# Optimization experiments

Measured on AMD Instinct MI355X. Metric: run time of the kernel, lower is better.

Reference implementation:

```python
import jax, jax.numpy as jnp
import numpy as np

N, E, D_IN, D_HID, D_OUT, R, B = 50000, 600000, 128, 128, 128, 8, 4


def setup_inputs() -> dict:
    key = jax.random.key(0)
    ks = jax.random.split(key, 12)
    s = 0.05
    return {
        "x": jax.random.normal(ks[0], (N, D_IN), jnp.float32),
        "edge_index": jax.random.randint(ks[1], (2, E), 0, N, jnp.int32),
        "edge_type": jax.random.randint(ks[2], (E,), 0, R, jnp.int32),
        "basis1": jax.random.normal(ks[3], (B, D_IN, D_HID), jnp.float32) * s,
        "comp1": jax.random.normal(ks[4], (R, B), jnp.float32) * s,
        "root1": jax.random.normal(ks[5], (D_IN, D_HID), jnp.float32) * s,
        "bias1": jnp.zeros((D_HID,), jnp.float32),
        "basis2": jax.random.normal(ks[6], (B, D_HID, D_OUT), jnp.float32) * s,
        "comp2": jax.random.normal(ks[7], (R, B), jnp.float32) * s,
        "root2": jax.random.normal(ks[8], (D_HID, D_OUT), jnp.float32) * s,
        "bias2": jnp.zeros((D_OUT,), jnp.float32),
    }


def _rgcn_conv(x, src, dst, etype, basis, comp, root, bias):
    # PyG RGCNConv (basis decomposition, aggr='mean' per relation):
    # out_i = x_i @ root + bias + sum_r mean_{e: type=r, dst=i} (x_src_e @ W_r)
    # W_r linear => aggregate raw features per (node, relation), then transform.
    n = x.shape[0]
    r = comp.shape[0]
    W = jnp.einsum('rb,bio->rio', comp, basis)          # [R, in, out]
    seg = dst * r + etype                               # [E] composite key
    agg = jax.ops.segment_sum(x[src], seg, num_segments=n * r)        # [N*R, in]
    cnt = jax.ops.segment_sum(jnp.ones_like(seg, x.dtype), seg, num_segments=n * r)
    mean = (agg / jnp.maximum(cnt, 1.0)[:, None]).reshape(n, r, -1)   # [N, R, in]
    return jnp.einsum('nri,rio->no', mean, W) + x @ root + bias


def reference(x, edge_index, edge_type, basis1, comp1, root1, bias1,
              basis2, comp2, root2, bias2):
    src, dst = edge_index[0], edge_index[1]
    h = _rgcn_conv(x, src, dst, edge_type, basis1, comp1, root1, bias1)
    h = jax.nn.relu(h)
    # dropout p=0.2 is identity in eval mode
    out = _rgcn_conv(h, src, dst, edge_type, basis2, comp2, root2, bias2)
    return out
```

## Files before the change

kernel.cpp:

```cpp
#include <hip/hip_runtime.h>

#define NN 50000
#define NE 600000
#define DD 128
#define RR 8
#define NBASIS 4
#define NR (NN * RR)
#define KTOT 640
#define KZ 512
#define MPAD 50048

typedef float f32x4 __attribute__((ext_vector_type(4)));
typedef short bf16x8 __attribute__((ext_vector_type(8)));
typedef unsigned int u32x4 __attribute__((ext_vector_type(4)));

static __device__ __forceinline__ unsigned short f2b(float f) {
  union { float f; unsigned u; } c; c.f = f;
  unsigned u = c.u + 0x7fffu + ((c.u >> 16) & 1u);
  return (unsigned short)(u >> 16);
}
static __device__ __forceinline__ unsigned pack2(float lo, float hi) {
  return (unsigned)f2b(lo) | ((unsigned)f2b(hi) << 16);
}
static __device__ __forceinline__ float b2f_lo(unsigned v) {
  union { unsigned u; float f; } c; c.u = v << 16; return c.f;
}
static __device__ __forceinline__ float b2f_hi(unsigned v) {
  union { unsigned u; float f; } c; c.u = v & 0xffff0000u; return c.f;
}

#define PREP_XB 12500
#define PREP_BT 320
#define PREP_CNT 2344
#define PREP_TOTAL (PREP_XB + 2 * PREP_BT + PREP_CNT)

__global__ __launch_bounds__(256) void prep_kernel(
    const float* __restrict__ x, const float* __restrict__ basis1,
    const float* __restrict__ root1, const float* __restrict__ basis2,
    const float* __restrict__ root2, const int* __restrict__ dst,
    const int* __restrict__ et, unsigned* __restrict__ xb,
    unsigned short* __restrict__ BT1, unsigned short* __restrict__ BT2,
    int* __restrict__ cnt) {
  int bid = blockIdx.x;
  int t = threadIdx.x;
  if (bid < PREP_XB) {
    int i = bid * 256 + t;
    float2 v = ((const float2*)x)[i];
    xb[i] = pack2(v.x, v.y);
  } else if (bid < PREP_XB + PREP_BT) {
    int idx = (bid - PREP_XB) * 256 + t;
    int c = idx / KTOT, k = idx - c * KTOT;
    float v = (k < 512) ? basis1[(size_t)((k >> 7) * DD + (k & 127)) * DD + c]
                        : root1[(size_t)(k - 512) * DD + c];
    BT1[idx] = f2b(v);
  } else if (bid < PREP_XB + 2 * PREP_BT) {
    int idx = (bid - PREP_XB - PREP_BT) * 256 + t;
    int c = idx / KTOT, k = idx - c * KTOT;
    float v = (k < 512) ? basis2[(size_t)((k >> 7) * DD + (k & 127)) * DD + c]
                        : root2[(size_t)(k - 512) * DD + c];
    BT2[idx] = f2b(v);
  } else {
    int e = (bid - PREP_XB - 2 * PREP_BT) * 256 + t;
    if (e < NE) atomicAdd(&cnt[dst[e] * RR + et[e]], 1);
  }
}

__global__ __launch_bounds__(256) void offs_kernel(
    const int* __restrict__ cnt, int2* __restrict__ od,
    int* __restrict__ curs, int* __restrict__ gcur) {
  __shared__ int s[256];
  __shared__ int base;
  int t = threadIdx.x;
  int i = blockIdx.x * 256 + t;
  int v = 0;
  if (i < NN) {
    const int4* c4 = (const int4*)cnt;
    int4 a = c4[i * 2];
    int4 b = c4[i * 2 + 1];
    v = a.x + a.y + a.z + a.w + b.x + b.y + b.z + b.w;
  }
  s[t] = v;
  __syncthreads();
  for (int off = 1; off < 256; off <<= 1) {
    int add = (t >= off) ? s[t - off] : 0;
    __syncthreads();
    s[t] += add;
    __syncthreads();
  }
  if (t == 255) base = atomicAdd(gcur, s[255]);
  __syncthreads();
  if (i < NN) {
    int o = base + s[t] - v;
    od[i] = make_int2(o, v);
    curs[i] = o;
  }
}

__global__ __launch_bounds__(256) void sort_kernel(
    const int* __restrict__ src, const int* __restrict__ dst,
    const int* __restrict__ et, int* __restrict__ curs,
    int* __restrict__ skey) {
  int e = blockIdx.x * 256 + threadIdx.x;
  if (e >= NE) return;
  int p = atomicAdd(&curs[dst[e]], 1);
  skey[p] = src[e] | (et[e] << 28);
}

__global__ __launch_bounds__(256) void agg_kernel(
    const u32x4* __restrict__ featb4,
    const int* __restrict__ skey, const int* __restrict__ cnt,
    const float* __restrict__ comp, const int2* __restrict__ od,
    u32x4* __restrict__ Ab4) {
  __shared__ float ccl[4][RR * NBASIS];
  int tid = threadIdx.x;
  int w = tid >> 6;
  int lane = tid & 63;
  int node = blockIdx.x * 4 + w;
  int g = lane >> 4;
  int q = lane & 15;

  int2 o_d = od[node];
  int beg = o_d.x, dg = o_d.y;

  if (lane < RR * NBASIS) {
    int c = cnt[node * RR + (lane >> 2)];
    ccl[w][lane] = comp[lane] * (1.0f / (float)max(c, 1));
  }
  __syncthreads();

  float a0[8] = {}, a1[8] = {}, a2[8] = {}, a3[8] = {};
  const float4* cc4 = (const float4*)ccl[w];

  for (int i = g; i < dg; i += 8) {
    int p0 = beg + i;
    bool has2 = (i + 4) < dg;
    int p1 = has2 ? p0 + 4 : p0;
    int k0 = skey[p0];
    int k1 = skey[p1];
    u32x4 v0 = featb4[(size_t)(k0 & 0x0FFFFFFF) * 16 + q];
    u32x4 v1 = featb4[(size_t)(k1 & 0x0FFFFFFF) * 16 + q];
    float4 c0 = cc4[((unsigned)k0) >> 28];
    float4 c1 = cc4[((unsigned)k1) >> 28];
    float s1 = has2 ? 1.f : 0.f;
    c1.x *= s1; c1.y *= s1; c1.z *= s1; c1.w *= s1;

    float e[8], f[8];
    e[0] = b2f_lo(v0.x); e[1] = b2f_hi(v0.x);
    e[2] = b2f_lo(v0.y); e[3] = b2f_hi(v0.y);
    e[4] = b2f_lo(v0.z); e[5] = b2f_hi(v0.z);
    e[6] = b2f_lo(v0.w); e[7] = b2f_hi(v0.w);
    f[0] = b2f_lo(v1.x); f[1] = b2f_hi(v1.x);
    f[2] = b2f_lo(v1.y); f[3] = b2f_hi(v1.y);
    f[4] = b2f_lo(v1.z); f[5] = b2f_hi(v1.z);
    f[6] = b2f_lo(v1.w); f[7] = b2f_hi(v1.w);
#pragma unroll
    for (int j = 0; j < 8; ++j) {
      a0[j] += c0.x * e[j] + c1.x * f[j];
      a1[j] += c0.y * e[j] + c1.y * f[j];
      a2[j] += c0.z * e[j] + c1.z * f[j];
      a3[j] += c0.w * e[j] + c1.w * f[j];
    }
  }

#pragma unroll
  for (int j = 0; j < 8; ++j) {
    a0[j] += __shfl_xor(a0[j], 16); a0[j] += __shfl_xor(a0[j], 32);
    a1[j] += __shfl_xor(a1[j], 16); a1[j] += __shfl_xor(a1[j], 32);
    a2[j] += __shfl_xor(a2[j], 16); a2[j] += __shfl_xor(a2[j], 32);
    a3[j] += __shfl_xor(a3[j], 16); a3[j] += __shfl_xor(a3[j], 32);
  }

  u32x4 wv;
  if (g == 0) {
    wv.x = pack2(a0[0], a0[1]); wv.y = pack2(a0[2], a0[3]);
    wv.z = pack2(a0[4], a0[5]); wv.w = pack2(a0[6], a0[7]);
  } else if (g == 1) {
    wv.x = pack2(a1[0], a1[1]); wv.y = pack2(a1[2], a1[3]);
    wv.z = pack2(a1[4], a1[5]); wv.w = pack2(a1[6], a1[7]);
  } else if (g == 2) {
    wv.x = pack2(a2[0], a2[1]); wv.y = pack2(a2[2], a2[3]);
    wv.z = pack2(a2[4], a2[5]); wv.w = pack2(a2[6], a2[7]);
  } else {
    wv.x = pack2(a3[0], a3[1]); wv.y = pack2(a3[2], a3[3]);
    wv.z = pack2(a3[4], a3[5]); wv.w = pack2(a3[6], a3[7]);
  }
  __builtin_nontemporal_store(wv, Ab4 + (size_t)node * 64 + g * 16 + q);
}

template <int OUT_BF16>
__global__ __launch_bounds__(256) void gemm_mfma(
    const unsigned short* __restrict__ Ab,
    const unsigned short* __restrict__ feat,
    const unsigned short* __restrict__ BT,
    const float* __restrict__ bias, void* __restrict__ Cout) {
  __shared__ unsigned short As[128][64];
  __shared__ unsigned short Bs[128][64];

  int tid = threadIdx.x;
  int row0 = blockIdx.x * 128;
  int lane = tid & 63;
  int wid = tid >> 6;
  int wr = (wid >> 1) * 64;
  int wc = (wid & 1) * 64;

  f32x4 acc[4][4] = {};

  for (int kt = 0; kt < KTOT; kt += 64) {
#pragma unroll
    for (int i = 0; i < 4; ++i) {
      int off = i * 256 + tid;
      int r = off >> 3;
      int ke = (off & 7) << 3;
      u32x4 av;
      if (kt < KZ)
        av = __builtin_nontemporal_load(
            (const u32x4*)(Ab + (size_t)(row0 + r) * KZ + kt + ke));
      else
        av = __builtin_nontemporal_load(
            (const u32x4*)(feat + (size_t)(row0 + r) * DD + (kt - KZ) + ke));
      *(u32x4*)((unsigned short*)As + (size_t)off * 8) = av;
      *(u32x4*)((unsigned short*)Bs + (size_t)off * 8) =
          *(const u32x4*)(BT + (size_t)r * KTOT + kt + ke);
    }
    __syncthreads();

#pragma unroll
    for (int kk = 0; kk < 2; ++kk) {
      int ko = kk * 32 + ((lane >> 4) << 3);
      bf16x8 a[4], b[4];
#pragma unroll
      for (int m = 0; m < 4; ++m)
        a[m] = *(const bf16x8*)&As[wr + m * 16 + (lane & 15)][ko];
#pragma unroll
      for (int n = 0; n < 4; ++n)
        b[n] = *(const bf16x8*)&Bs[wc + n * 16 + (lane & 15)][ko];
#pragma unroll
      for (int m = 0; m < 4; ++m)
#pragma unroll
        for (int n = 0; n < 4; ++n)
          acc[m][n] = __builtin_amdgcn_mfma_f32_16x16x32_bf16(
              a[m], b[n], acc[m][n], 0, 0, 0);
    }
    __syncthreads();
  }

#pragma unroll
  for (int n = 0; n < 4; ++n) {
    int col = wc + n * 16 + (lane & 15);
    float bb = bias[col];
#pragma unroll
    for (int m = 0; m < 4; ++m) {
      f32x4 v = acc[m][n];
#pragma unroll
      for (int j = 0; j < 4; ++j) {
        int row = row0 + wr + m * 16 + ((lane >> 4) << 2) + j;
        if (row < NN) {
          float o = v[j] + bb;
          if (OUT_BF16) {
            o = fmaxf(o, 0.f);
            ((unsigned short*)Cout)[(size_t)row * DD + col] = f2b(o);
          } else {
            ((float*)Cout)[(size_t)row * DD + col] = o;
          }
        }
      }
    }
  }
}

extern "C" void kernel_launch(void* const* d_in, const int* in_sizes, int n_in,
                              void* d_out, int out_size, void* d_ws,
                              size_t ws_size, hipStream_t stream) {
  const float* x      = (const float*)d_in[0];
  const int*   eidx   = (const int*)d_in[1];
  const int*   etype  = (const int*)d_in[2];
  const float* basis1 = (const float*)d_in[3];
  const float* comp1  = (const float*)d_in[4];
  const float* root1  = (const float*)d_in[5];
  const float* bias1  = (const float*)d_in[6];
  const float* basis2 = (const float*)d_in[7];
  const float* comp2  = (const float*)d_in[8];
  const float* root2  = (const float*)d_in[9];
  const float* bias2  = (const float*)d_in[10];
  float* out = (float*)d_out;

  const int* src = eidx;
  const int* dst = eidx + NE;

  unsigned short* Ab  = (unsigned short*)d_ws;
  unsigned short* xb  = Ab + (size_t)MPAD * KZ;
  unsigned short* hb  = xb + (size_t)MPAD * DD;
  unsigned short* BT1 = hb + (size_t)MPAD * DD;
  unsigned short* BT2 = BT1 + (size_t)DD * KTOT;
  int*  skey = (int*)(BT2 + (size_t)DD * KTOT);
  int*  cnt  = skey + NE;
  int*  gcur = cnt + NR;
  int2* od   = (int2*)(gcur + 4);
  int*  curs = (int*)(od + NN);

  const int NB = (NN + 255) / 256;
  const int EB = (NE + 255) / 256;

  hipMemsetAsync(cnt, 0, (size_t)(NR + 4) * sizeof(int), stream);
  prep_kernel<<<PREP_TOTAL, 256, 0, stream>>>(
      x, basis1, root1, basis2, root2, dst, etype, (unsigned*)xb, BT1, BT2,
      cnt);
  offs_kernel<<<NB, 256, 0, stream>>>(cnt, od, curs, gcur);
  sort_kernel<<<EB, 256, 0, stream>>>(src, dst, etype, curs, skey);

  int agg_blocks = NN / 4;
  int gemm_blocks = MPAD / 128;

  agg_kernel<<<agg_blocks, 256, 0, stream>>>((const u32x4*)xb, skey, cnt,
                                             comp1, od, (u32x4*)Ab);
  gemm_mfma<1><<<gemm_blocks, 256, 0, stream>>>(Ab, xb, BT1, bias1, hb);
  agg_kernel<<<agg_blocks, 256, 0, stream>>>((const u32x4*)hb, skey, cnt,
                                             comp2, od, (u32x4*)Ab);
  gemm_mfma<0><<<gemm_blocks, 256, 0, stream>>>(Ab, hb, BT2, bias2, out);
}
```

Measured before the change: 250.7 us.

## Split neighbor aggregation into two feature-half passes to shrink gather working set

Result: slower. 361.5 us (+44.2%).

```diff
diff --git a/kernel.cpp b/kernel.cpp
--- a/kernel.cpp
+++ b/kernel.cpp
@@ -106,18 +106,19 @@
   skey[p] = src[e] | (et[e] << 28);
 }
 
-__global__ __launch_bounds__(256) void agg_kernel(
+__global__ __launch_bounds__(256) void agg_half_kernel(
     const u32x4* __restrict__ featb4,
     const int* __restrict__ skey, const int* __restrict__ cnt,
     const float* __restrict__ comp, const int2* __restrict__ od,
-    u32x4* __restrict__ Ab4) {
+    u32x4* __restrict__ Ab4,
+    int half) {
   __shared__ float ccl[4][RR * NBASIS];
   int tid = threadIdx.x;
   int w = tid >> 6;
   int lane = tid & 63;
   int node = blockIdx.x * 4 + w;
-  int g = lane >> 4;
-  int q = lane & 15;
+  int g = lane >> 3;
+  int q = lane & 7;
 
   int2 o_d = od[node];
   int beg = o_d.x, dg = o_d.y;
@@ -130,18 +131,19 @@
 
   float a0[8] = {}, a1[8] = {}, a2[8] = {}, a3[8] = {};
   const float4* cc4 = (const float4*)ccl[w];
-
-  for (int i = g; i < dg; i += 8) {
+  const u32x4* fb = featb4 + half * 8 + q;
+
+  for (int i = g; i < dg; i += 16) {
     int p0 = beg + i;
-    bool has2 = (i + 4) < dg;
-    int p1 = has2 ? p0 + 4 : p0;
+    bool h1 = (i + 8) < dg;
+    int p1 = h1 ? p0 + 8 : p0;
     int k0 = skey[p0];
     int k1 = skey[p1];
-    u32x4 v0 = featb4[(size_t)(k0 & 0x0FFFFFFF) * 16 + q];
-    u32x4 v1 = featb4[(size_t)(k1 & 0x0FFFFFFF) * 16 + q];
+    u32x4 v0 = fb[(size_t)(k0 & 0x0FFFFFFF) * 16];
+    u32x4 v1 = fb[(size_t)(k1 & 0x0FFFFFFF) * 16];
     float4 c0 = cc4[((unsigned)k0) >> 28];
     float4 c1 = cc4[((unsigned)k1) >> 28];
-    float s1 = has2 ? 1.f : 0.f;
+    float s1 = h1 ? 1.f : 0.f;
     c1.x *= s1; c1.y *= s1; c1.z *= s1; c1.w *= s1;
 
     float e[8], f[8];
@@ -164,27 +166,34 @@
 
 #pragma unroll
   for (int j = 0; j < 8; ++j) {
-    a0[j] += __shfl_xor(a0[j], 16); a0[j] += __shfl_xor(a0[j], 32);
-    a1[j] += __shfl_xor(a1[j], 16); a1[j] += __shfl_xor(a1[j], 32);
-    a2[j] += __shfl_xor(a2[j], 16); a2[j] += __shfl_xor(a2[j], 32);
-    a3[j] += __shfl_xor(a3[j], 16); a3[j] += __shfl_xor(a3[j], 32);
-  }
-
-  u32x4 wv;
-  if (g == 0) {
-    wv.x = pack2(a0[0], a0[1]); wv.y = pack2(a0[2], a0[3]);
-    wv.z = pack2(a0[4], a0[5]); wv.w = pack2(a0[6], a0[7]);
-  } else if (g == 1) {
-    wv.x = pack2(a1[0], a1[1]); wv.y = pack2(a1[2], a1[3]);
-    wv.z = pack2(a1[4], a1[5]); wv.w = pack2(a1[6], a1[7]);
-  } else if (g == 2) {
-    wv.x = pack2(a2[0], a2[1]); wv.y = pack2(a2[2], a2[3]);
-    wv.z = pack2(a2[4], a2[5]); wv.w = pack2(a2[6], a2[7]);
-  } else {
-    wv.x = pack2(a3[0], a3[1]); wv.y = pack2(a3[2], a3[3]);
-    wv.z = pack2(a3[4], a3[5]); wv.w = pack2(a3[6], a3[7]);
-  }
-  __builtin_nontemporal_store(wv, Ab4 + (size_t)node * 64 + g * 16 + q);
+    a0[j] += __shfl_xor(a0[j], 8);  a0[j] += __shfl_xor(a0[j], 16);
+    a0[j] += __shfl_xor(a0[j], 32);
+    a1[j] += __shfl_xor(a1[j], 8);  a1[j] += __shfl_xor(a1[j], 16);
+    a1[j] += __shfl_xor(a1[j], 32);
+    a2[j] += __shfl_xor(a2[j], 8);  a2[j] += __shfl_xor(a2[j], 16);
+    a2[j] += __shfl_xor(a2[j], 32);
+    a3[j] += __shfl_xor(a3[j], 8);  a3[j] += __shfl_xor(a3[j], 16);
+    a3[j] += __shfl_xor(a3[j], 32);
+  }
+
+  if (lane < 32) {
+    u32x4 wv;
+    if (g == 0) {
+      wv.x = pack2(a0[0], a0[1]); wv.y = pack2(a0[2], a0[3]);
+      wv.z = pack2(a0[4], a0[5]); wv.w = pack2(a0[6], a0[7]);
+    } else if (g == 1) {
+      wv.x = pack2(a1[0], a1[1]); wv.y = pack2(a1[2], a1[3]);
+      wv.z = pack2(a1[4], a1[5]); wv.w = pack2(a1[6], a1[7]);
+    } else if (g == 2) {
+      wv.x = pack2(a2[0], a2[1]); wv.y = pack2(a2[2], a2[3]);
+      wv.z = pack2(a2[4], a2[5]); wv.w = pack2(a2[6], a2[7]);
+    } else {
+      wv.x = pack2(a3[0], a3[1]); wv.y = pack2(a3[2], a3[3]);
+      wv.z = pack2(a3[4], a3[5]); wv.w = pack2(a3[6], a3[7]);
+    }
+    __builtin_nontemporal_store(
+        wv, Ab4 + (size_t)node * 64 + g * 16 + half * 8 + q);
+  }
 }
 
 template <int OUT_BF16>
@@ -216,8 +225,7 @@
         av = __builtin_nontemporal_load(
             (const u32x4*)(Ab + (size_t)(row0 + r) * KZ + kt + ke));
       else
-        av = __builtin_nontemporal_load(
-            (const u32x4*)(feat + (size_t)(row0 + r) * DD + (kt - KZ) + ke));
+        av = *(const u32x4*)(feat + (size_t)(row0 + r) * DD + (kt - KZ) + ke);
       *(u32x4*)((unsigned short*)As + (size_t)off * 8) = av;
       *(u32x4*)((unsigned short*)Bs + (size_t)off * 8) =
           *(const u32x4*)(BT + (size_t)r * KTOT + kt + ke);
@@ -311,10 +319,14 @@
   int agg_blocks = NN / 4;
   int gemm_blocks = MPAD / 128;
 
-  agg_kernel<<<agg_blocks, 256, 0, stream>>>((const u32x4*)xb, skey, cnt,
-                                             comp1, od, (u32x4*)Ab);
+  agg_half_kernel<<<agg_blocks, 256, 0, stream>>>(
+      (const u32x4*)xb, skey, cnt, comp1, od, (u32x4*)Ab, 0);
+  agg_half_kernel<<<agg_blocks, 256, 0, stream>>>(
+      (const u32x4*)xb, skey, cnt, comp1, od, (u32x4*)Ab, 1);
   gemm_mfma<1><<<gemm_blocks, 256, 0, stream>>>(Ab, xb, BT1, bias1, hb);
-  agg_kernel<<<agg_blocks, 256, 0, stream>>>((const u32x4*)hb, skey, cnt,
-                                             comp2, od, (u32x4*)Ab);
+  agg_half_kernel<<<agg_blocks, 256, 0, stream>>>(
+      (const u32x4*)hb, skey, cnt, comp2, od, (u32x4*)Ab, 0);
+  agg_half_kernel<<<agg_blocks, 256, 0, stream>>>(
+      (const u32x4*)hb, skey, cnt, comp2, od, (u32x4*)Ab, 1);
   gemm_mfma<0><<<gemm_blocks, 256, 0, stream>>>(Ab, hb, BT2, bias2, out);
 }
```

## Process two nodes per wave in aggregation with upfront prefetched gathers

Applied to the files above, without the earlier changes.

Result: faster. 232.5 us, median of 2 (-7.2%).

```diff
diff --git a/kernel.cpp b/kernel.cpp
--- a/kernel.cpp
+++ b/kernel.cpp
@@ -9,6 +9,7 @@
 #define KTOT 640
 #define KZ 512
 #define MPAD 50048
+#define KMASK 0x0FFFFFFF
 
 typedef float f32x4 __attribute__((ext_vector_type(4)));
 typedef short bf16x8 __attribute__((ext_vector_type(8)));
@@ -27,6 +28,22 @@
 }
 static __device__ __forceinline__ float b2f_hi(unsigned v) {
   union { unsigned u; float f; } c; c.u = v & 0xffff0000u; return c.f;
+}
+
+static __device__ __forceinline__ void fma8(float* a0, float* a1, float* a2,
+                                            float* a3, u32x4 v, float4 c) {
+  float e[8];
+  e[0] = b2f_lo(v.x); e[1] = b2f_hi(v.x);
+  e[2] = b2f_lo(v.y); e[3] = b2f_hi(v.y);
+  e[4] = b2f_lo(v.z); e[5] = b2f_hi(v.z);
+  e[6] = b2f_lo(v.w); e[7] = b2f_hi(v.w);
+#pragma unroll
+  for (int j = 0; j < 8; ++j) {
+    a0[j] += c.x * e[j];
+    a1[j] += c.y * e[j];
+    a2[j] += c.z * e[j];
+    a3[j] += c.w * e[j];
+  }
 }
 
 #define PREP_XB 12500
@@ -111,80 +128,168 @@
     const int* __restrict__ skey, const int* __restrict__ cnt,
     const float* __restrict__ comp, const int2* __restrict__ od,
     u32x4* __restrict__ Ab4) {
-  __shared__ float ccl[4][RR * NBASIS];
+  __shared__ float ccl[8][RR * NBASIS];
   int tid = threadIdx.x;
   int w = tid >> 6;
   int lane = tid & 63;
-  int node = blockIdx.x * 4 + w;
+  int nA = blockIdx.x * 8 + w * 2;
+  int nB = nA + 1;
   int g = lane >> 4;
   int q = lane & 15;
 
-  int2 o_d = od[node];
-  int beg = o_d.x, dg = o_d.y;
-
-  if (lane < RR * NBASIS) {
-    int c = cnt[node * RR + (lane >> 2)];
-    ccl[w][lane] = comp[lane] * (1.0f / (float)max(c, 1));
+  {
+    int which = lane >> 5;
+    int idx = lane & 31;
+    int node = nA + which;
+    int c = cnt[node * RR + (idx >> 2)];
+    ccl[w * 2 + which][idx] = comp[idx] * (1.0f / (float)max(c, 1));
   }
   __syncthreads();
 
+  int2 odA = od[nA];
+  int2 odB = od[nB];
+  int begA = odA.x, dgA = odA.y;
+  int begB = odB.x, dgB = odB.y;
+  int lastA = min(begA + max(dgA, 1) - 1, NE - 1);
+  int lastB = min(begB + max(dgB, 1) - 1, NE - 1);
+
+  int pA0 = min(begA + g, lastA);
+  int pA1 = min(begA + g + 4, lastA);
+  int pA2 = min(begA + g + 8, lastA);
+  int kA0 = skey[pA0], kA1 = skey[pA1], kA2 = skey[pA2];
+  u32x4 vA0 = featb4[(size_t)(kA0 & KMASK) * 16 + q];
+  u32x4 vA1 = featb4[(size_t)(kA1 & KMASK) * 16 + q];
+  u32x4 vA2 = featb4[(size_t)(kA2 & KMASK) * 16 + q];
+
+  int pB0 = min(begB + g, lastB);
+  int pB1 = min(begB + g + 4, lastB);
+  int pB2 = min(begB + g + 8, lastB);
+  int kB0 = skey[pB0], kB1 = skey[pB1], kB2 = skey[pB2];
+  u32x4 vB0 = featb4[(size_t)(kB0 & KMASK) * 16 + q];
+  u32x4 vB1 = featb4[(size_t)(kB1 & KMASK) * 16 + q];
+  u32x4 vB2 = featb4[(size_t)(kB2 & KMASK) * 16 + q];
+
   float a0[8] = {}, a1[8] = {}, a2[8] = {}, a3[8] = {};
-  const float4* cc4 = (const float4*)ccl[w];
-
-  for (int i = g; i < dg; i += 8) {
-    int p0 = beg + i;
-    bool has2 = (i + 4) < dg;
-    int p1 = has2 ? p0 + 4 : p0;
-    int k0 = skey[p0];
-    int k1 = skey[p1];
-    u32x4 v0 = featb4[(size_t)(k0 & 0x0FFFFFFF) * 16 + q];
-    u32x4 v1 = featb4[(size_t)(k1 & 0x0FFFFFFF) * 16 + q];
-    float4 c0 = cc4[((unsigned)k0) >> 28];
-    float4 c1 = cc4[((unsigned)k1) >> 28];
-    float s1 = has2 ? 1.f : 0.f;
+
+  {
+    const float4* cc4 = (const float4*)ccl[w * 2];
+    float4 c0 = cc4[((unsigned)kA0) >> 28];
+    float4 c1 = cc4[((unsigned)kA1) >> 28];
+    float4 c2 = cc4[((unsigned)kA2) >> 28];
+    float s0 = (g < dgA) ? 1.f : 0.f;
+    float s1 = (g + 4 < dgA) ? 1.f : 0.f;
+    float s2 = (g + 8 < dgA) ? 1.f : 0.f;
+    c0.x *= s0; c0.y *= s0; c0.z *= s0; c0.w *= s0;
     c1.x *= s1; c1.y *= s1; c1.z *= s1; c1.w *= s1;
-
-    float e[8], f[8];
-    e[0] = b2f_lo(v0.x); e[1] = b2f_hi(v0.x);
-    e[2] = b2f_lo(v0.y); e[3] = b2f_hi(v0.y);
-    e[4] = b2f_lo(v0.z); e[5] = b2f_hi(v0.z);
-    e[6] = b2f_lo(v0.w); e[7] = b2f_hi(v0.w);
-    f[0] = b2f_lo(v1.x); f[1] = b2f_hi(v1.x);
-    f[2] = b2f_lo(v1.y); f[3] = b2f_hi(v1.y);
-    f[4] = b2f_lo(v1.z); f[5] = b2f_hi(v1.z);
-    f[6] = b2f_lo(v1.w); f[7] = b2f_hi(v1.w);
+    c2.x *= s2; c2.y *= s2; c2.z *= s2; c2.w *= s2;
+    fma8(a0, a1, a2, a3, vA0, c0);
+    fma8(a0, a1, a2, a3, vA1, c1);
+    fma8(a0, a1, a2, a3, vA2, c2);
+
+    for (int i = g + 12; i < dgA; i += 12) {
+      int p0 = begA + i;
+      int p1 = min(p0 + 4, lastA);
+      int p2 = min(p0 + 8, lastA);
+      int k0 = skey[p0], k1 = skey[p1], k2 = skey[p2];
+      u32x4 v0 = featb4[(size_t)(k0 & KMASK) * 16 + q];
+      u32x4 v1 = featb4[(size_t)(k1 & KMASK) * 16 + q];
+      u32x4 v2 = featb4[(size_t)(k2 & KMASK) * 16 + q];
+      float4 c0t = cc4[((unsigned)k0) >> 28];
+      float4 c1t = cc4[((unsigned)k1) >> 28];
+      float4 c2t = cc4[((unsigned)k2) >> 28];
+      float t1 = (i + 4 < dgA) ? 1.f : 0.f;
+      float t2 = (i + 8 < dgA) ? 1.f : 0.f;
+      c1t.x *= t1; c1t.y *= t1; c1t.z *= t1; c1t.w *= t1;
+      c2t.x *= t2; c2t.y *= t2; c2t.z *= t2; c2t.w *= t2;
+      fma8(a0, a1, a2, a3, v0, c0t);
+      fma8(a0, a1, a2, a3, v1, c1t);
+      fma8(a0, a1, a2, a3, v2, c2t);
+    }
+
 #pragma unroll
     for (int j = 0; j < 8; ++j) {
-      a0[j] += c0.x * e[j] + c1.x * f[j];
-      a1[j] += c0.y * e[j] + c1.y * f[j];
-      a2[j] += c0.z * e[j] + c1.z * f[j];
-      a3[j] += c0.w * e[j] + c1.w * f[j];
-    }
-  }
-
-#pragma unroll
-  for (int j = 0; j < 8; ++j) {
-    a0[j] += __shfl_xor(a0[j], 16); a0[j] += __shfl_xor(a0[j], 32);
-    a1[j] += __shfl_xor(a1[j], 16); a1[j] += __shfl_xor(a1[j], 32);
-    a2[j] += __shfl_xor(a2[j], 16); a2[j] += __shfl_xor(a2[j], 32);
-    a3[j] += __shfl_xor(a3[j], 16); a3[j] += __shfl_xor(a3[j], 32);
-  }
-
-  u32x4 wv;
-  if (g == 0) {
-    wv.x = pack2(a0[0], a0[1]); wv.y = pack2(a0[2], a0[3]);
-    wv.z = pack2(a0[4], a0[5]); wv.w = pack2(a0[6], a0[7]);
-  } else if (g == 1) {
-    wv.x = pack2(a1[0], a1[1]); wv.y = pack2(a1[2], a1[3]);
-    wv.z = pack2(a1[4], a1[5]); wv.w = pack2(a1[6], a1[7]);
-  } else if (g == 2) {
-    wv.x = pack2(a2[0], a2[1]); wv.y = pack2(a2[2], a2[3]);
-    wv.z = pack2(a2[4], a2[5]); wv.w = pack2(a2[6], a2[7]);
-  } else {
-    wv.x = pack2(a3[0], a3[1]); wv.y = pack2(a3[2], a3[3]);
-    wv.z = pack2(a3[4], a3[5]); wv.w = pack2(a3[6], a3[7]);
-  }
-  __builtin_nontemporal_store(wv, Ab4 + (size_t)node * 64 + g * 16 + q);
+      a0[j] += __shfl_xor(a0[j], 16); a0[j] += __shfl_xor(a0[j], 32);
+      a1[j] += __shfl_xor(a1[j], 16); a1[j] += __shfl_xor(a1[j], 32);
+      a2[j] += __shfl_xor(a2[j], 16); a2[j] += __shfl_xor(a2[j], 32);
+      a3[j] += __shfl_xor(a3[j], 16); a3[j] += __shfl_xor(a3[j], 32);
+    }
+    u32x4 wv;
+    if (g == 0) {
+      wv.x = pack2(a0[0], a0[1]); wv.y = pack2(a0[2], a0[3]);
+      wv.z = pack2(a0[4], a0[5]); wv.w = pack2(a0[6], a0[7]);
+    } else if (g == 1) {
+      wv.x = pack2(a1[0], a1[1]); wv.y = pack2(a1[2], a1[3]);
+      wv.z = pack2(a1[4], a1[5]); wv.w = pack2(a1[6], a1[7]);
+    } else if (g == 2) {
+      wv.x = pack2(a2[0], a2[1]); wv.y = pack2(a2[2], a2[3]);
+      wv.z = pack2(a2[4], a2[5]); wv.w = pack2(a2[6], a2[7]);
+    } else {
+      wv.x = pack2(a3[0], a3[1]); wv.y = pack2(a3[2], a3[3]);
+      wv.z = pack2(a3[4], a3[5]); wv.w = pack2(a3[6], a3[7]);
+    }
+    __builtin_nontemporal_store(wv, Ab4 + (size_t)nA * 64 + g * 16 + q);
+  }
+
+  {
+#pragma unroll
+    for (int j = 0; j < 8; ++j) { a0[j] = 0.f; a1[j] = 0.f; a2[j] = 0.f; a3[j] = 0.f; }
+    const float4* cc4 = (const float4*)ccl[w * 2 + 1];
+    float4 c0 = cc4[((unsigned)kB0) >> 28];
+    float4 c1 = cc4[((unsigned)kB1) >> 28];
+    float4 c2 = cc4[((unsigned)kB2) >> 28];
+    float s0 = (g < dgB) ? 1.f : 0.f;
+    float s1 = (g + 4 < dgB) ? 1.f : 0.f;
+    float s2 = (g + 8 < dgB) ? 1.f : 0.f;
+    c0.x *= s0; c0.y *= s0; c0.z *= s0; c0.w *= s0;
+    c1.x *= s1; c1.y *= s1; c1.z *= s1; c1.w *= s1;
+    c2.x *= s2; c2.y *= s2; c2.z *= s2; c2.w *= s2;
+    fma8(a0, a1, a2, a3, vB0, c0);
+    fma8(a0, a1, a2, a3, vB1, c1);
+    fma8(a0, a1, a2, a3, vB2, c2);
+
+    for (int i = g + 12; i < dgB; i += 12) {
+      int p0 = begB + i;
+      int p1 = min(p0 + 4, lastB);
+      int p2 = min(p0 + 8, lastB);
+      int k0 = skey[p0], k1 = skey[p1], k2 = skey[p2];
+      u32x4 v0 = featb4[(size_t)(k0 & KMASK) * 16 + q];
+      u32x4 v1 = featb4[(size_t)(k1 & KMASK) * 16 + q];
+      u32x4 v2 = featb4[(size_t)(k2 & KMASK) * 16 + q];
+      float4 c0t = cc4[((unsigned)k0) >> 28];
+      float4 c1t = cc4[((unsigned)k1) >> 28];
+      float4 c2t = cc4[((unsigned)k2) >> 28];
+      float t1 = (i + 4 < dgB) ? 1.f : 0.f;
+      float t2 = (i + 8 < dgB) ? 1.f : 0.f;
+      c1t.x *= t1; c1t.y *= t1; c1t.z *= t1; c1t.w *= t1;
+      c2t.x *= t2; c2t.y *= t2; c2t.z *= t2; c2t.w *= t2;
+      fma8(a0, a1, a2, a3, v0, c0t);
+      fma8(a0, a1, a2, a3, v1, c1t);
+      fma8(a0, a1, a2, a3, v2, c2t);
+    }
+
+#pragma unroll
+    for (int j = 0; j < 8; ++j) {
+      a0[j] += __shfl_xor(a0[j], 16); a0[j] += __shfl_xor(a0[j], 32);
+      a1[j] += __shfl_xor(a1[j], 16); a1[j] += __shfl_xor(a1[j], 32);
+      a2[j] += __shfl_xor(a2[j], 16); a2[j] += __shfl_xor(a2[j], 32);
+      a3[j] += __shfl_xor(a3[j], 16); a3[j] += __shfl_xor(a3[j], 32);
+    }
+    u32x4 wv;
+    if (g == 0) {
+      wv.x = pack2(a0[0], a0[1]); wv.y = pack2(a0[2], a0[3]);
+      wv.z = pack2(a0[4], a0[5]); wv.w = pack2(a0[6], a0[7]);
+    } else if (g == 1) {
+      wv.x = pack2(a1[0], a1[1]); wv.y = pack2(a1[2], a1[3]);
+      wv.z = pack2(a1[4], a1[5]); wv.w = pack2(a1[6], a1[7]);
+    } else if (g == 2) {
+      wv.x = pack2(a2[0], a2[1]); wv.y = pack2(a2[2], a2[3]);
+      wv.z = pack2(a2[4], a2[5]); wv.w = pack2(a2[6], a2[7]);
+    } else {
+      wv.x = pack2(a3[0], a3[1]); wv.y = pack2(a3[2], a3[3]);
+      wv.z = pack2(a3[4], a3[5]); wv.w = pack2(a3[6], a3[7]);
+    }
+    __builtin_nontemporal_store(wv, Ab4 + (size_t)nB * 64 + g * 16 + q);
+  }
 }
 
 template <int OUT_BF16>
@@ -216,8 +321,7 @@
         av = __builtin_nontemporal_load(
             (const u32x4*)(Ab + (size_t)(row0 + r) * KZ + kt + ke));
       else
-        av = __builtin_nontemporal_load(
-            (const u32x4*)(feat + (size_t)(row0 + r) * DD + (kt - KZ) + ke));
+        av = *(const u32x4*)(feat + (size_t)(row0 + r) * DD + (kt - KZ) + ke);
       *(u32x4*)((unsigned short*)As + (size_t)off * 8) = av;
       *(u32x4*)((unsigned short*)Bs + (size_t)off * 8) =
           *(const u32x4*)(BT + (size_t)r * KTOT + kt + ke);
@@ -308,7 +412,7 @@
   offs_kernel<<<NB, 256, 0, stream>>>(cnt, od, curs, gcur);
   sort_kernel<<<EB, 256, 0, stream>>>(src, dst, etype, curs, skey);
 
-  int agg_blocks = NN / 4;
+  int agg_blocks = NN / 8;
   int gemm_blocks = MPAD / 128;
 
   agg_kernel<<<agg_blocks, 256, 0, stream>>>((const u32x4*)xb, skey, cnt,
```
